# Performance work log

Hardware: AMD Instinct MI355X
Metric: run time of the kernel (lower is better)

The kernel has to match this reference:

```python
import jax, jax.numpy as jnp
import numpy as np

# ROI / grid constants (from cfg)
X_MIN, Y_MIN, Z_MIN = 0.0, -16.0, -2.0
X_MAX, Y_MAX, Z_MAX = 72.0, 16.0, 7.6
VX = VY = VZ = 0.2
NX = int(round((X_MAX - X_MIN) / VX))  # 360
NY = int(round((Y_MAX - Y_MIN) / VY))  # 160
NZ = int(round((Z_MAX - Z_MIN) / VZ))  # 48
C = 4  # input_dim
B = 8
N_PTS = 1_600_000


def setup_inputs() -> dict:
    key = jax.random.key(0)
    k1, k2, k3 = jax.random.split(key, 3)
    # points uniformly inside ROI: (x, y, z, power)
    u = jax.random.uniform(k1, (N_PTS, 3), dtype=jnp.float32)
    lo = jnp.array([X_MIN, Y_MIN, Z_MIN], jnp.float32)
    hi = jnp.array([X_MAX, Y_MAX, Z_MAX], jnp.float32)
    xyz = lo + u * (hi - lo)
    power = jax.random.normal(k2, (N_PTS, 1), dtype=jnp.float32)
    rdr_sparse = jnp.concatenate([xyz, power], axis=-1)  # [N, 4]
    batch_indices = jnp.sort(jax.random.randint(k3, (N_PTS,), 0, B, dtype=jnp.int64))
    return {"rdr_sparse": rdr_sparse, "batch_indices": batch_indices, "batch_size": B}


def reference(rdr_sparse, batch_indices, batch_size):
    """Point-to-voxel (max 1 pt/voxel, first point wins) + sparse->dense scatter.
    Returns dense_input of shape [B, C, Z, Y, X], matching spconv .dense()."""
    n = rdr_sparse.shape[0]
    pts = rdr_sparse[:, :3]
    lo = jnp.array([X_MIN, Y_MIN, Z_MIN], rdr_sparse.dtype)
    vsz = jnp.array([VX, VY, VZ], rdr_sparse.dtype)
    vox = jnp.floor((pts - lo) / vsz).astype(jnp.int32)  # (xi, yi, zi)
    xi, yi, zi = vox[:, 0], vox[:, 1], vox[:, 2]
    valid = (xi >= 0) & (xi < NX) & (yi >= 0) & (yi < NY) & (zi >= 0) & (zi < NZ)
    b = batch_indices.astype(jnp.int32)
    G = batch_size * NZ * NY * NX
    flat = ((b * NZ + zi) * NY + yi) * NX + xi          # [N]
    flat = jnp.where(valid, flat, G)                     # dump invalid pts in slot G
    pid = jnp.arange(n, dtype=jnp.int32)
    winner = jnp.full((G + 1,), n, jnp.int32).at[flat].min(pid)  # [G+1]
    # gather winning features; index n -> zero row (empty voxel)
    feats_pad = jnp.concatenate(
        [rdr_sparse, jnp.zeros((1, C), rdr_sparse.dtype)], axis=0)  # [N+1, C]
    dense_flat = feats_pad[winner[:G]]                   # [G, C]
    dense = dense_flat.reshape(batch_size, NZ, NY, NX, C)
    dense = jnp.transpose(dense, (0, 4, 1, 2, 3))        # [B, C, Z, Y, X]
    return dense
```

## Files before the change

kernel.cpp:

```cpp
#include <hip/hip_runtime.h>

#define VNX 360
#define VNY 160
#define VNZ 48
#define VC 4
static constexpr int PLANE = VNZ * VNY * VNX;

typedef unsigned int u32x4 __attribute__((ext_vector_type(4)));
typedef float        f32x4 __attribute__((ext_vector_type(4)));

__global__ void vox_init_kernel(u32x4* __restrict__ w4, int n4) {
    int stride = gridDim.x * blockDim.x;
    u32x4 s = { ~0u, ~0u, ~0u, ~0u };
    for (int t = blockIdx.x * blockDim.x + threadIdx.x; t < n4; t += stride)
        w4[t] = s;
}

__global__ void vox_points_kernel(const float4* __restrict__ pts,
                                  const int* __restrict__ bidx,
                                  unsigned int* __restrict__ winner,
                                  int n) {
    int i = blockIdx.x * blockDim.x + threadIdx.x;
    if (i >= n) return;

    float4 p = pts[i];
    int xi = (int)floorf((p.x -  0.0f) * 5.0f);
    int yi = (int)floorf((p.y + 16.0f) * 5.0f);
    int zi = (int)floorf((p.z +  2.0f) * 5.0f);

    if ((unsigned)xi >= VNX || (unsigned)yi >= VNY || (unsigned)zi >= VNZ)
        return;

    int b = bidx[i];
    int flat = ((b * VNZ + zi) * VNY + yi) * VNX + xi;
    atomicMin(&winner[flat], (unsigned int)i);
}

__global__ void vox_gather_kernel(const u32x4* __restrict__ winner4,
                                  const f32x4* __restrict__ feats,
                                  float* __restrict__ out,
                                  unsigned int n, int nvox4) {
    int stride = gridDim.x * blockDim.x;
    const f32x4 zero = { 0.f, 0.f, 0.f, 0.f };

    for (int t = blockIdx.x * blockDim.x + threadIdx.x; t < nvox4; t += stride) {
        u32x4 w = __builtin_nontemporal_load(&winner4[t]);

        f32x4 f0 = (w.x < n) ? feats[w.x] : zero;
        f32x4 f1 = (w.y < n) ? feats[w.y] : zero;
        f32x4 f2 = (w.z < n) ? feats[w.z] : zero;
        f32x4 f3 = (w.w < n) ? feats[w.w] : zero;

        int v = t * 4;
        int b = v / PLANE;
        int r = v - b * PLANE;
        float* base = out + (size_t)b * (VC * (size_t)PLANE) + r;

        f32x4 c0 = { f0.x, f1.x, f2.x, f3.x };
        f32x4 c1 = { f0.y, f1.y, f2.y, f3.y };
        f32x4 c2 = { f0.z, f1.z, f2.z, f3.z };
        f32x4 c3 = { f0.w, f1.w, f2.w, f3.w };
        __builtin_nontemporal_store(c0, (f32x4*)(base + 0 * (size_t)PLANE));
        __builtin_nontemporal_store(c1, (f32x4*)(base + 1 * (size_t)PLANE));
        __builtin_nontemporal_store(c2, (f32x4*)(base + 2 * (size_t)PLANE));
        __builtin_nontemporal_store(c3, (f32x4*)(base + 3 * (size_t)PLANE));
    }
}

extern "C" void kernel_launch(void* const* d_in, const int* in_sizes, int n_in,
                              void* d_out, int out_size, void* d_ws, size_t ws_size,
                              hipStream_t stream) {
    const float* rdr  = (const float*)d_in[0];
    const int*   bidx = (const int*)d_in[1];
    int n = in_sizes[1];

    int G     = out_size / VC;
    int n4    = G / 4;

    unsigned int* winner = (unsigned int*)d_ws;

    int block = 256;
    int grid_dense = 2048;

    vox_init_kernel<<<grid_dense, block, 0, stream>>>((u32x4*)winner, n4);

    vox_points_kernel<<<(n + block - 1) / block, block, 0, stream>>>(
        (const float4*)rdr, bidx, winner, n);

    vox_gather_kernel<<<grid_dense, block, 0, stream>>>(
        (const u32x4*)winner, (const f32x4*)rdr, (float*)d_out,
        (unsigned int)n, n4);
}
```

Before: 162.2 us.

## Fuse init, scatter and gather into one cooperative kernel with per-batch overlap

New measurement: 610.4 us. +276.2%, slower.

```diff
diff --git a/kernel.cpp b/kernel.cpp
--- a/kernel.cpp
+++ b/kernel.cpp
@@ -1,93 +1,155 @@
 #include <hip/hip_runtime.h>
+#include <hip/hip_cooperative_groups.h>
+
+namespace cg = cooperative_groups;
 
 #define VNX 360
 #define VNY 160
 #define VNZ 48
 #define VC 4
-static constexpr int PLANE = VNZ * VNY * VNX;
+static constexpr int PLANE  = VNZ * VNY * VNX;
+static constexpr int NBATCH = 8;
+static constexpr int NTH    = 256;
+static constexpr int NBLK   = 1024;
+static constexpr int NBP    = 256;
+static constexpr int NBG    = NBLK - NBP;
+static constexpr int GTOT   = NBATCH * PLANE;
+static constexpr int G4     = GTOT / 4;
+static constexpr int TAIL4  = 345600;
+static constexpr int SPLIT4 = G4 - TAIL4;
 
 typedef unsigned int u32x4 __attribute__((ext_vector_type(4)));
 typedef float        f32x4 __attribute__((ext_vector_type(4)));
 
-__global__ void vox_init_kernel(u32x4* __restrict__ w4, int n4) {
-    int stride = gridDim.x * blockDim.x;
-    u32x4 s = { ~0u, ~0u, ~0u, ~0u };
-    for (int t = blockIdx.x * blockDim.x + threadIdx.x; t < n4; t += stride)
-        w4[t] = s;
+struct Ctrl {
+    unsigned int done[NBATCH];
+    int          bnd[NBATCH + 1];
+};
+
+__device__ __forceinline__ void gather_group(
+        const unsigned int* __restrict__ winner,
+        const f32x4* __restrict__ feats,
+        float* __restrict__ out, unsigned int n, int g)
+{
+    u32x4 w = __builtin_nontemporal_load((const u32x4*)winner + g);
+    const f32x4 zero = {0.f, 0.f, 0.f, 0.f};
+    f32x4 f0 = (w.x < n) ? feats[w.x] : zero;
+    f32x4 f1 = (w.y < n) ? feats[w.y] : zero;
+    f32x4 f2 = (w.z < n) ? feats[w.z] : zero;
+    f32x4 f3 = (w.w < n) ? feats[w.w] : zero;
+
+    int v = g * 4;
+    int b = v / PLANE;
+    int r = v - b * PLANE;
+    float* base = out + (size_t)b * (VC * (size_t)PLANE) + r;
+
+    f32x4 c0 = {f0.x, f1.x, f2.x, f3.x};
+    f32x4 c1 = {f0.y, f1.y, f2.y, f3.y};
+    f32x4 c2 = {f0.z, f1.z, f2.z, f3.z};
+    f32x4 c3 = {f0.w, f1.w, f2.w, f3.w};
+    __builtin_nontemporal_store(c0, (f32x4*)(base + 0 * (size_t)PLANE));
+    __builtin_nontemporal_store(c1, (f32x4*)(base + 1 * (size_t)PLANE));
+    __builtin_nontemporal_store(c2, (f32x4*)(base + 2 * (size_t)PLANE));
+    __builtin_nontemporal_store(c3, (f32x4*)(base + 3 * (size_t)PLANE));
 }
 
-__global__ void vox_points_kernel(const float4* __restrict__ pts,
-                                  const int* __restrict__ bidx,
-                                  unsigned int* __restrict__ winner,
-                                  int n) {
-    int i = blockIdx.x * blockDim.x + threadIdx.x;
-    if (i >= n) return;
-
-    float4 p = pts[i];
-    int xi = (int)floorf((p.x -  0.0f) * 5.0f);
-    int yi = (int)floorf((p.y + 16.0f) * 5.0f);
-    int zi = (int)floorf((p.z +  2.0f) * 5.0f);
-
-    if ((unsigned)xi >= VNX || (unsigned)yi >= VNY || (unsigned)zi >= VNZ)
-        return;
-
-    int b = bidx[i];
-    int flat = ((b * VNZ + zi) * VNY + yi) * VNX + xi;
-    atomicMin(&winner[flat], (unsigned int)i);
+__device__ __forceinline__ void wait_batch(Ctrl* ctl, int b) {
+    if (threadIdx.x == 0) {
+        while (__hip_atomic_load(&ctl->done[b], __ATOMIC_RELAXED,
+                                 __HIP_MEMORY_SCOPE_AGENT) < (unsigned)NBP)
+            __builtin_amdgcn_s_sleep(16);
+    }
+    __syncthreads();
+    __builtin_amdgcn_fence(__ATOMIC_ACQUIRE, "agent");
 }
 
-__global__ void vox_gather_kernel(const u32x4* __restrict__ winner4,
-                                  const f32x4* __restrict__ feats,
-                                  float* __restrict__ out,
-                                  unsigned int n, int nvox4) {
-    int stride = gridDim.x * blockDim.x;
-    const f32x4 zero = { 0.f, 0.f, 0.f, 0.f };
+__global__ __launch_bounds__(NTH, 4)
+void vox_fused(const f32x4* __restrict__ pts,
+               const int*   __restrict__ bidx,
+               unsigned int* __restrict__ winner,
+               Ctrl*        __restrict__ ctl,
+               float*       __restrict__ out,
+               int n)
+{
+    const int blk = blockIdx.x, tid = threadIdx.x;
 
-    for (int t = blockIdx.x * blockDim.x + threadIdx.x; t < nvox4; t += stride) {
-        u32x4 w = __builtin_nontemporal_load(&winner4[t]);
+    {
+        u32x4 s = {~0u, ~0u, ~0u, ~0u};
+        u32x4* w4 = (u32x4*)winner;
+        for (int t = blk * NTH + tid; t < G4; t += NBLK * NTH)
+            w4[t] = s;
+    }
+    if (blk == 0) {
+        if (tid < NBATCH) {
+            __hip_atomic_store(&ctl->done[tid], 0u, __ATOMIC_RELAXED,
+                               __HIP_MEMORY_SCOPE_AGENT);
+        } else if (tid >= 32 && tid < 32 + NBATCH + 1) {
+            int b = tid - 32;
+            int lo = 0, hi = n;
+            if (b == 0)            { lo = 0; }
+            else if (b == NBATCH)  { lo = n; }
+            else {
+                while (lo < hi) { int m = (lo + hi) >> 1;
+                                  if (bidx[m] < b) lo = m + 1; else hi = m; }
+            }
+            ctl->bnd[b] = lo;
+        }
+    }
+    cg::this_grid().sync();
 
-        f32x4 f0 = (w.x < n) ? feats[w.x] : zero;
-        f32x4 f1 = (w.y < n) ? feats[w.y] : zero;
-        f32x4 f2 = (w.z < n) ? feats[w.z] : zero;
-        f32x4 f3 = (w.w < n) ? feats[w.w] : zero;
+    const unsigned int un = (unsigned int)n;
 
-        int v = t * 4;
-        int b = v / PLANE;
-        int r = v - b * PLANE;
-        float* base = out + (size_t)b * (VC * (size_t)PLANE) + r;
-
-        f32x4 c0 = { f0.x, f1.x, f2.x, f3.x };
-        f32x4 c1 = { f0.y, f1.y, f2.y, f3.y };
-        f32x4 c2 = { f0.z, f1.z, f2.z, f3.z };
-        f32x4 c3 = { f0.w, f1.w, f2.w, f3.w };
-        __builtin_nontemporal_store(c0, (f32x4*)(base + 0 * (size_t)PLANE));
-        __builtin_nontemporal_store(c1, (f32x4*)(base + 1 * (size_t)PLANE));
-        __builtin_nontemporal_store(c2, (f32x4*)(base + 2 * (size_t)PLANE));
-        __builtin_nontemporal_store(c3, (f32x4*)(base + 3 * (size_t)PLANE));
+    if (blk < NBP) {
+        for (int b = 0; b < NBATCH; ++b) {
+            int lo = ctl->bnd[b], hi = ctl->bnd[b + 1];
+            for (int i = lo + blk * NTH + tid; i < hi; i += NBP * NTH) {
+                f32x4 p = pts[i];
+                int xi = (int)floorf((p.x -  0.0f) * 5.0f);
+                int yi = (int)floorf((p.y + 16.0f) * 5.0f);
+                int zi = (int)floorf((p.z +  2.0f) * 5.0f);
+                if ((unsigned)xi < VNX && (unsigned)yi < VNY && (unsigned)zi < VNZ) {
+                    int flat = ((b * VNZ + zi) * VNY + yi) * VNX + xi;
+                    atomicMin(&winner[flat], (unsigned int)i);
+                }
+            }
+            __syncthreads();
+            if (tid == 0)
+                __hip_atomic_fetch_add(&ctl->done[b], 1u, __ATOMIC_RELEASE,
+                                       __HIP_MEMORY_SCOPE_AGENT);
+        }
+        wait_batch(ctl, NBATCH - 1);
+        for (int g = SPLIT4 + blk * NTH + tid; g < G4; g += NBP * NTH)
+            gather_group(winner, pts, out, un, g);
+    } else {
+        const int gj = blk - NBP;
+        int cur_ready = -1;
+        for (long g0 = (long)gj * NTH; g0 < SPLIT4; g0 += (long)NBG * NTH) {
+            long gm = g0 + NTH - 1; if (gm > SPLIT4 - 1) gm = SPLIT4 - 1;
+            int bneed = (int)((gm * 4) / PLANE);
+            if (bneed > cur_ready) {
+                wait_batch(ctl, bneed);
+                cur_ready = bneed;
+            }
+            int g = (int)g0 + tid;
+            if (g < SPLIT4)
+                gather_group(winner, pts, out, un, g);
+        }
     }
 }
 
 extern "C" void kernel_launch(void* const* d_in, const int* in_sizes, int n_in,
                               void* d_out, int out_size, void* d_ws, size_t ws_size,
                               hipStream_t stream) {
-    const float* rdr  = (const float*)d_in[0];
+    const f32x4* pts  = (const f32x4*)d_in[0];
     const int*   bidx = (const int*)d_in[1];
     int n = in_sizes[1];
 
-    int G     = out_size / VC;
-    int n4    = G / 4;
+    unsigned int* winner = (unsigned int*)d_ws;
+    Ctrl* ctl = (Ctrl*)((char*)d_ws + (size_t)GTOT * 4);
+    float* out = (float*)d_out;
 
-    unsigned int* winner = (unsigned int*)d_ws;
-
-    int block = 256;
-    int grid_dense = 2048;
-
-    vox_init_kernel<<<grid_dense, block, 0, stream>>>((u32x4*)winner, n4);
-
-    vox_points_kernel<<<(n + block - 1) / block, block, 0, stream>>>(
-        (const float4*)rdr, bidx, winner, n);
-
-    vox_gather_kernel<<<grid_dense, block, 0, stream>>>(
-        (const u32x4*)winner, (const f32x4*)rdr, (float*)d_out,
-        (unsigned int)n, n4);
+    void* args[] = { (void*)&pts, (void*)&bidx, (void*)&winner,
+                     (void*)&ctl, (void*)&out, (void*)&n };
+    hipLaunchCooperativeKernel((const void*)vox_fused,
+                               dim3(NBLK), dim3(NTH), args, 0, stream);
 }
```
